# Kernel tuning notes

Measured on AMD Instinct MI355X. Metric: run time of the kernel, lower is better.

Reference implementation:

```python
import jax, jax.numpy as jnp
import numpy as np

BIGINT = 1e10
BOA, BOH, BOL = 21, 22, 23      # global-node residue symbols
ATOM_POS_PAD = 0                # atom position pad index
AG_SEG = 1                      # antigen segment id


def setup_inputs() -> dict:
    key = jax.random.key(0)
    ks = jax.random.split(key, 8)
    B, L, C, E = 16, 128, 14, 256
    N = B * L
    # residues with global tokens at fixed positions per protein
    S = jax.random.randint(ks[0], (B, L), 0, 21)
    S = S.at[:, 0].set(BOA).at[:, 48].set(BOH).at[:, 96].set(BOL)
    S = S.reshape(N)
    seg = np.zeros((L,), np.int32); seg[0:48] = 1; seg[48:96] = 2; seg[96:] = 3
    segment_ids = jnp.tile(jnp.asarray(seg), B)
    RP = jnp.tile(jnp.arange(L, dtype=jnp.int32), B)
    A = jax.random.randint(ks[1], (N, C), 1, 16)
    AP = jax.random.randint(ks[2], (N, C), 0, 16)
    AP = AP.at[:, :4].set(jnp.arange(1, 5, dtype=AP.dtype)[None, :])  # backbone always present
    X = jax.random.normal(ks[3], (N, C, 3), dtype=jnp.float32) * 3.0
    res_embed = jax.random.normal(ks[4], (25, E), dtype=jnp.float32) * 0.02
    atom_embed = jax.random.normal(ks[5], (16, E), dtype=jnp.float32) * 0.02
    atom_pos_embed = jax.random.normal(ks[6], (16, E), dtype=jnp.float32) * 0.02
    return dict(S=S, RP=RP, A=A, AP=AP, X=X, segment_ids=segment_ids,
                res_embed=res_embed, atom_embed=atom_embed,
                atom_pos_embed=atom_pos_embed, max_n=L, k_neighbors=9)


def _embed(S, RP, A, AP, res_embed, atom_embed, atom_pos_embed):
    N = S.shape[0]
    E = res_embed.shape[1]
    half = E // 2
    inv = jnp.power(10000.0, -2.0 * jnp.arange(half, dtype=jnp.float32) / E)
    ang = RP.astype(jnp.float32)[:, None] * inv[None, :]
    pos_e = jnp.stack([jnp.sin(ang), jnp.cos(ang)], axis=-1).reshape(N, E)
    res_e = res_embed[S] + pos_e
    atom_e = atom_embed[A] + atom_pos_embed[AP]            # [N,C,E]
    not_pad = (AP != ATOM_POS_PAD)
    denom = not_pad.sum(-1, keepdims=True).astype(res_e.dtype) + 1e-10
    atom_e = jnp.sum(atom_e * not_pad[..., None], axis=1) / denom
    return jnp.concatenate([res_e, atom_e], axis=-1)       # [N,2E]


def _min_pair_dist(X, AP, max_n):
    # min over atom pairs of ||X[i,a]-X[j,b]||, pad atoms pushed to BIGINT
    N, C, _ = X.shape
    B = N // max_n
    Xb = X.reshape(B, max_n, C, 3)
    pad = (AP == ATOM_POS_PAD).reshape(B, max_n, C)
    sq = jnp.sum(Xb * Xb, axis=-1)                          # [B,L,C]
    dot = jnp.einsum('biad,bjcd->biajc', Xb, Xb)            # [B,L,C,L,C]
    d2 = sq[:, :, :, None, None] + sq[:, None, None, :, :] - 2.0 * dot
    dist = jnp.sqrt(jnp.maximum(d2, 0.0))
    pmask = pad[:, :, :, None, None] | pad[:, None, None, :, :]
    dist = dist + pmask.astype(dist.dtype) * BIGINT
    return jnp.min(dist, axis=(2, 4))                       # [B,L,L]


def _knn(dist_mat, sel_mask, k):
    # smallest-k neighbors among selected candidate edges; invalid -> -1
    B, L, _ = dist_mat.shape
    d = jnp.where(sel_mask, dist_mat, BIGINT)
    neg, dst_local = jax.lax.top_k(-d, k)                   # [B,L,k]
    valid = ((-neg) < BIGINT).reshape(-1)
    offs = (jnp.arange(B) * L)[:, None, None]
    src = jnp.broadcast_to(jnp.arange(L)[None, :, None] + offs, (B, L, k)).reshape(-1)
    dst = (dst_local + offs).reshape(-1)
    src = jnp.where(valid, src, -1)
    dst = jnp.where(valid, dst, -1)
    return jnp.stack([src, dst]), valid


def reference(S, RP, A, AP, X, segment_ids, res_embed, atom_embed, atom_pos_embed, max_n, k_neighbors):
    N = S.shape[0]
    L = max_n
    B = N // L
    h = _embed(S, RP, A, AP, res_embed, atom_embed, atom_pos_embed)
    dist = _min_pair_dist(X, AP, L)                          # [B,L,L]
    g = ((S == BOA) | (S == BOH) | (S == BOL)).reshape(B, L)
    seg = segment_ids.reshape(B, L)
    not_self = ~jnp.eye(L, dtype=bool)[None]                 # exclude i==j
    gi, gj = g[:, :, None], g[:, None, :]
    not_global = ~(gi | gj)
    same_seg = seg[:, :, None] == seg[:, None, :]
    inner_mask = same_seg & not_global & not_self
    outer_mask = (~same_seg) & not_global & not_self
    ctx_knn, ctx_valid = _knn(dist, inner_mask, k_neighbors)
    inter_knn, inter_valid = _knn(dist, outer_mask, k_neighbors)
    # non-kNN ctx edges (global_normal | global_global | sequential), dense adjacency
    global_normal = same_seg & (gi | gj) & not_self
    global_global = gi & gj & not_self
    idx = jnp.arange(L)
    adj_seq = (jnp.abs(idx[:, None] - idx[None, :]) == 1)[None]
    seq_mask = adj_seq & not_global & (seg[:, :, None] != AG_SEG)
    extra_ctx_adj = global_normal | global_global | seq_mask  # [B,L,L] bool
    return h, ctx_knn, ctx_valid, extra_ctx_adj, inter_knn, inter_valid
```

## Files before the change

kernel.cpp:

```cpp
#include <hip/hip_runtime.h>
#include <math.h>
#include <float.h>
#include <stdint.h>

#define BIGINT_F 1e10f
#define L_TOK 128
#define C_ATOM 14
#define E_DIM 256
#define K_NB 9

__device__ __forceinline__ float sq3(float x, float y, float z) {
    return __fadd_rn(__fadd_rn(__fmul_rn(x, x), __fmul_rn(y, y)), __fmul_rn(z, z));
}

__device__ __forceinline__ uint64_t umin64(uint64_t a, uint64_t b) { return a < b ? a : b; }

__global__ void __launch_bounds__(256)
fused_kernel(const int* __restrict__ S, const int* __restrict__ RP,
             const int* __restrict__ A, const int* __restrict__ AP,
             const float* __restrict__ X, const int* __restrict__ seg,
             const float* __restrict__ res_embed,
             const float* __restrict__ atom_embed,
             const float* __restrict__ atom_pos_embed,
             float* __restrict__ h,
             float* __restrict__ ctx_src, float* __restrict__ ctx_dst, float* __restrict__ ctx_val,
             float* __restrict__ adj_out,
             float* __restrict__ int_src, float* __restrict__ int_dst, float* __restrict__ int_val,
             int N) {
    const int NKNN = N / 4;
    int blk = blockIdx.x;
    int tid = threadIdx.x;

    if (blk < NKNN) {
        int wave = tid >> 6;
        int lane = tid & 63;
        int bi = blk * 4 + wave;
        int b  = bi >> 7;
        int i  = bi & (L_TOK - 1);

        __shared__ float4 sxi[4][C_ATOM];
        if (lane < C_ATOM) {
            const float* xp = X + ((size_t)bi * C_ATOM + lane) * 3;
            float x0 = xp[0], x1 = xp[1], x2 = xp[2];
            float sq = (AP[bi * C_ATOM + lane] == 0) ? INFINITY : sq3(x0, x1, x2);
            sxi[wave][lane] = make_float4(x0, x1, x2, sq);
        }
        __syncthreads();

        float xa0[C_ATOM], xa1[C_ATOM], xa2[C_ATOM], sa[C_ATOM];
        #pragma unroll
        for (int a = 0; a < C_ATOM; ++a) {
            float4 t = sxi[wave][a];
            xa0[a] = t.x; xa1[a] = t.y; xa2[a] = t.z; sa[a] = t.w;
        }

        int j0 = lane, j1 = lane + 64;
        int nj0 = (b << 7) + j0, nj1 = (b << 7) + j1;

        float mind0 = INFINITY, mind1 = INFINITY;
        for (int c = 0; c < C_ATOM; ++c) {
            const float* yp0 = X + ((size_t)nj0 * C_ATOM + c) * 3;
            const float* yp1 = X + ((size_t)nj1 * C_ATOM + c) * 3;
            float y00 = yp0[0], y01 = yp0[1], y02 = yp0[2];
            float y10 = yp1[0], y11 = yp1[1], y12 = yp1[2];
            float sc0 = (AP[nj0 * C_ATOM + c] == 0) ? INFINITY : sq3(y00, y01, y02);
            float sc1 = (AP[nj1 * C_ATOM + c] == 0) ? INFINITY : sq3(y10, y11, y12);
            #pragma unroll
            for (int a = 0; a < C_ATOM; ++a) {
                float dot0 = __fadd_rn(__fadd_rn(__fmul_rn(xa0[a], y00),
                                                 __fmul_rn(xa1[a], y01)),
                                       __fmul_rn(xa2[a], y02));
                float d20 = __fsub_rn(__fadd_rn(sa[a], sc0), __fmul_rn(2.0f, dot0));
                mind0 = fminf(mind0, d20);
                float dot1 = __fadd_rn(__fadd_rn(__fmul_rn(xa0[a], y10),
                                                 __fmul_rn(xa1[a], y11)),
                                       __fmul_rn(xa2[a], y12));
                float d21 = __fsub_rn(__fadd_rn(sa[a], sc1), __fmul_rn(2.0f, dot1));
                mind1 = fminf(mind1, d21);
            }
        }
        float d0 = sqrtf(fmaxf(mind0, 0.0f));
        float d1 = sqrtf(fmaxf(mind1, 0.0f));

        int si = S[bi];
        int segi = seg[bi];
        bool gi = si >= 21;
        int sj0 = S[nj0], sj1 = S[nj1];
        int segj0 = seg[nj0], segj1 = seg[nj1];
        bool gj0 = sj0 >= 21, gj1 = sj1 >= 21;
        bool ng0 = !gi && !gj0 && (j0 != i);
        bool ng1 = !gi && !gj1 && (j1 != i);
        bool inner0 = (segi == segj0) && ng0;
        bool inner1 = (segi == segj1) && ng1;
        bool outer0 = (segi != segj0) && ng0;
        bool outer1 = (segi != segj1) && ng1;

        const uint32_t bigbits = __float_as_uint(BIGINT_F);
        uint64_t kd0 = ((uint64_t)__float_as_uint(d0) << 32) | (uint32_t)j0;
        uint64_t kd1 = ((uint64_t)__float_as_uint(d1) << 32) | (uint32_t)j1;
        uint64_t kbig0 = ((uint64_t)bigbits << 32) | (uint32_t)j0;
        uint64_t kbig1 = ((uint64_t)bigbits << 32) | (uint32_t)j1;

        for (int pass = 0; pass < 2; ++pass) {
            uint64_t k0 = (pass == 0 ? inner0 : outer0) ? kd0 : kbig0;
            uint64_t k1 = (pass == 0 ? inner1 : outer1) ? kd1 : kbig1;
            float* osrc = (pass == 0) ? ctx_src : int_src;
            float* odst = (pass == 0) ? ctx_dst : int_dst;
            float* oval = (pass == 0) ? ctx_val : int_val;
            #pragma unroll
            for (int k = 0; k < K_NB; ++k) {
                uint64_t kk = umin64(k0, k1);
                #pragma unroll
                for (int m = 32; m > 0; m >>= 1) {
                    uint64_t o = __shfl_xor((unsigned long long)kk, m, 64);
                    kk = umin64(kk, o);
                }
                if (k0 == kk) k0 = UINT64_MAX;
                if (k1 == kk) k1 = UINT64_MAX;
                if (lane == 0) {
                    uint32_t dbits = (uint32_t)(kk >> 32);
                    int jmin = (int)(uint32_t)kk;
                    bool valid = dbits < bigbits;
                    int o = bi * K_NB + k;
                    osrc[o] = valid ? (float)bi : -1.0f;
                    odst[o] = valid ? (float)((b << 7) + jmin) : -1.0f;
                    oval[o] = valid ? 1.0f : 0.0f;
                }
            }
        }
    } else if (blk < NKNN + N) {
        int n = blk - NKNN;
        int e = tid;
        int s = S[n];
        float rp = (float)RP[n];

        int k = e >> 1;
        const float c1 = (float)(-2.0 * 13.287712379549449 / (double)E_DIM);
        float invk = exp2f((float)k * c1);
        float ang = rp * invk;
        float pe = (e & 1) ? cosf(ang) : sinf(ang);
        h[(size_t)n * (2 * E_DIM) + e] = res_embed[s * E_DIM + e] + pe;

        __shared__ int sA[C_ATOM], sAP[C_ATOM];
        if (e < C_ATOM) { sA[e] = A[n * C_ATOM + e]; sAP[e] = AP[n * C_ATOM + e]; }
        __syncthreads();

        float sum = 0.0f, cnt = 0.0f;
        for (int c = 0; c < C_ATOM; ++c) {
            if (sAP[c] != 0) {
                sum += atom_embed[sA[c] * E_DIM + e] + atom_pos_embed[sAP[c] * E_DIM + e];
                cnt += 1.0f;
            }
        }
        h[(size_t)n * (2 * E_DIM) + E_DIM + e] = sum / (cnt + 1e-10f);
    } else {
        int idx = (blk - NKNN - N) * 256 + tid;
        int b = idx >> 14;
        int i = (idx >> 7) & (L_TOK - 1);
        int j = idx & (L_TOK - 1);
        int ni = (b << 7) + i, nj = (b << 7) + j;
        bool gi = S[ni] >= 21, gj = S[nj] >= 21;
        int segi = seg[ni], segj = seg[nj];
        bool notself = (i != j);
        bool same = (segi == segj);
        bool gn = same && (gi || gj) && notself;
        bool gg = gi && gj && notself;
        int d = i - j;
        bool adjacent = (d == 1 || d == -1);
        bool sm = adjacent && !(gi || gj) && (segi != 1);
        adj_out[idx] = (gn || gg || sm) ? 1.0f : 0.0f;
    }
}

extern "C" void kernel_launch(void* const* d_in, const int* in_sizes, int n_in,
                              void* d_out, int out_size, void* d_ws, size_t ws_size,
                              hipStream_t stream) {
    const int*   S    = (const int*)d_in[0];
    const int*   RP   = (const int*)d_in[1];
    const int*   A    = (const int*)d_in[2];
    const int*   AP   = (const int*)d_in[3];
    const float* X    = (const float*)d_in[4];
    const int*   seg  = (const int*)d_in[5];
    const float* rese = (const float*)d_in[6];
    const float* atme = (const float*)d_in[7];
    const float* atpe = (const float*)d_in[8];

    const int N = in_sizes[0];
    const int B = N / L_TOK;
    float* out = (float*)d_out;

    size_t off = 0;
    float* h_out   = out + off;  off += (size_t)N * 2 * E_DIM;
    float* ctx_src = out + off;  off += (size_t)N * K_NB;
    float* ctx_dst = out + off;  off += (size_t)N * K_NB;
    float* ctx_val = out + off;  off += (size_t)N * K_NB;
    float* adj_out = out + off;  off += (size_t)B * L_TOK * L_TOK;
    float* int_src = out + off;  off += (size_t)N * K_NB;
    float* int_dst = out + off;  off += (size_t)N * K_NB;
    float* int_val = out + off;  off += (size_t)N * K_NB;

    int nknn = N / 4;
    int nadj = (B * L_TOK * L_TOK) / 256;
    int grid = nknn + N + nadj;
    fused_kernel<<<grid, 256, 0, stream>>>(S, RP, A, AP, X, seg, rese, atme, atpe,
                                           h_out, ctx_src, ctx_dst, ctx_val,
                                           adj_out, int_src, int_dst, int_val, N);
}
```

Before: 97.65 us.

## Replace 64-bit shuffle top-k with DPP float min, ballot argmin, interleaved passes

The k-nearest-neighbour selection drops the packed 64-bit key and xor-shuffle reduction in favour of a 32-bit float wave minimum built from DPP row operations, plus readlane and ballot/ctz to find the lowest lane holding that minimum. The inner and outer selections now run interleaved in one loop, and each lane keeps its k-th result so the outputs go out in one coalesced store instead of lane-0 scalar writes. It also folds the -2 factor into the cached query coordinates to save a multiply per atom pair. Ties now break by lane with the j0 half checked before j1, which still picks the lowest index. Entries with non-finite distances get a reconstructed index instead of the old packed one, but those rows are marked invalid anyway.

```diff
diff --git a/kernel.cpp b/kernel.cpp
--- a/kernel.cpp
+++ b/kernel.cpp
@@ -13,7 +13,19 @@
     return __fadd_rn(__fadd_rn(__fmul_rn(x, x), __fmul_rn(y, y)), __fmul_rn(z, z));
 }
 
-__device__ __forceinline__ uint64_t umin64(uint64_t a, uint64_t b) { return a < b ? a : b; }
+__device__ __forceinline__ float wave_min63(float v) {
+#define DPP_MIN(ctrl)                                                         \
+    v = fminf(v, __int_as_float(__builtin_amdgcn_update_dpp(                  \
+            __float_as_int(v), __float_as_int(v), (ctrl), 0xf, 0xf, false)));
+    DPP_MIN(0x111)
+    DPP_MIN(0x112)
+    DPP_MIN(0x114)
+    DPP_MIN(0x118)
+    DPP_MIN(0x142)
+    DPP_MIN(0x143)
+#undef DPP_MIN
+    return v;
+}
 
 __global__ void __launch_bounds__(256)
 fused_kernel(const int* __restrict__ S, const int* __restrict__ RP,
@@ -37,46 +49,47 @@
         int bi = blk * 4 + wave;
         int b  = bi >> 7;
         int i  = bi & (L_TOK - 1);
+        const float INF_F = __int_as_float(0x7f800000);
 
         __shared__ float4 sxi[4][C_ATOM];
         if (lane < C_ATOM) {
             const float* xp = X + ((size_t)bi * C_ATOM + lane) * 3;
             float x0 = xp[0], x1 = xp[1], x2 = xp[2];
-            float sq = (AP[bi * C_ATOM + lane] == 0) ? INFINITY : sq3(x0, x1, x2);
-            sxi[wave][lane] = make_float4(x0, x1, x2, sq);
+            float sq = (AP[bi * C_ATOM + lane] == 0) ? INF_F : sq3(x0, x1, x2);
+            sxi[wave][lane] = make_float4(__fmul_rn(x0, -2.0f),
+                                          __fmul_rn(x1, -2.0f),
+                                          __fmul_rn(x2, -2.0f), sq);
         }
         __syncthreads();
 
-        float xa0[C_ATOM], xa1[C_ATOM], xa2[C_ATOM], sa[C_ATOM];
+        float za0[C_ATOM], za1[C_ATOM], za2[C_ATOM], sa[C_ATOM];
         #pragma unroll
         for (int a = 0; a < C_ATOM; ++a) {
             float4 t = sxi[wave][a];
-            xa0[a] = t.x; xa1[a] = t.y; xa2[a] = t.z; sa[a] = t.w;
+            za0[a] = t.x; za1[a] = t.y; za2[a] = t.z; sa[a] = t.w;
         }
 
         int j0 = lane, j1 = lane + 64;
         int nj0 = (b << 7) + j0, nj1 = (b << 7) + j1;
 
-        float mind0 = INFINITY, mind1 = INFINITY;
+        float mind0 = INF_F, mind1 = INF_F;
         for (int c = 0; c < C_ATOM; ++c) {
             const float* yp0 = X + ((size_t)nj0 * C_ATOM + c) * 3;
             const float* yp1 = X + ((size_t)nj1 * C_ATOM + c) * 3;
             float y00 = yp0[0], y01 = yp0[1], y02 = yp0[2];
             float y10 = yp1[0], y11 = yp1[1], y12 = yp1[2];
-            float sc0 = (AP[nj0 * C_ATOM + c] == 0) ? INFINITY : sq3(y00, y01, y02);
-            float sc1 = (AP[nj1 * C_ATOM + c] == 0) ? INFINITY : sq3(y10, y11, y12);
+            float sc0 = (AP[nj0 * C_ATOM + c] == 0) ? INF_F : sq3(y00, y01, y02);
+            float sc1 = (AP[nj1 * C_ATOM + c] == 0) ? INF_F : sq3(y10, y11, y12);
             #pragma unroll
             for (int a = 0; a < C_ATOM; ++a) {
-                float dot0 = __fadd_rn(__fadd_rn(__fmul_rn(xa0[a], y00),
-                                                 __fmul_rn(xa1[a], y01)),
-                                       __fmul_rn(xa2[a], y02));
-                float d20 = __fsub_rn(__fadd_rn(sa[a], sc0), __fmul_rn(2.0f, dot0));
-                mind0 = fminf(mind0, d20);
-                float dot1 = __fadd_rn(__fadd_rn(__fmul_rn(xa0[a], y10),
-                                                 __fmul_rn(xa1[a], y11)),
-                                       __fmul_rn(xa2[a], y12));
-                float d21 = __fsub_rn(__fadd_rn(sa[a], sc1), __fmul_rn(2.0f, dot1));
-                mind1 = fminf(mind1, d21);
+                float t0 = __fadd_rn(__fadd_rn(__fmul_rn(za0[a], y00),
+                                               __fmul_rn(za1[a], y01)),
+                                     __fmul_rn(za2[a], y02));
+                mind0 = fminf(mind0, __fadd_rn(__fadd_rn(sa[a], sc0), t0));
+                float t1 = __fadd_rn(__fadd_rn(__fmul_rn(za0[a], y10),
+                                               __fmul_rn(za1[a], y11)),
+                                     __fmul_rn(za2[a], y12));
+                mind1 = fminf(mind1, __fadd_rn(__fadd_rn(sa[a], sc1), t1));
             }
         }
         float d0 = sqrtf(fmaxf(mind0, 0.0f));
@@ -95,38 +108,62 @@
         bool outer0 = (segi != segj0) && ng0;
         bool outer1 = (segi != segj1) && ng1;
 
-        const uint32_t bigbits = __float_as_uint(BIGINT_F);
-        uint64_t kd0 = ((uint64_t)__float_as_uint(d0) << 32) | (uint32_t)j0;
-        uint64_t kd1 = ((uint64_t)__float_as_uint(d1) << 32) | (uint32_t)j1;
-        uint64_t kbig0 = ((uint64_t)bigbits << 32) | (uint32_t)j0;
-        uint64_t kbig1 = ((uint64_t)bigbits << 32) | (uint32_t)j1;
-
-        for (int pass = 0; pass < 2; ++pass) {
-            uint64_t k0 = (pass == 0 ? inner0 : outer0) ? kd0 : kbig0;
-            uint64_t k1 = (pass == 0 ? inner1 : outer1) ? kd1 : kbig1;
-            float* osrc = (pass == 0) ? ctx_src : int_src;
-            float* odst = (pass == 0) ? ctx_dst : int_dst;
-            float* oval = (pass == 0) ? ctx_val : int_val;
-            #pragma unroll
-            for (int k = 0; k < K_NB; ++k) {
-                uint64_t kk = umin64(k0, k1);
-                #pragma unroll
-                for (int m = 32; m > 0; m >>= 1) {
-                    uint64_t o = __shfl_xor((unsigned long long)kk, m, 64);
-                    kk = umin64(kk, o);
-                }
-                if (k0 == kk) k0 = UINT64_MAX;
-                if (k1 == kk) k1 = UINT64_MAX;
-                if (lane == 0) {
-                    uint32_t dbits = (uint32_t)(kk >> 32);
-                    int jmin = (int)(uint32_t)kk;
-                    bool valid = dbits < bigbits;
-                    int o = bi * K_NB + k;
-                    osrc[o] = valid ? (float)bi : -1.0f;
-                    odst[o] = valid ? (float)((b << 7) + jmin) : -1.0f;
-                    oval[o] = valid ? 1.0f : 0.0f;
-                }
-            }
+        float cA0 = inner0 ? d0 : INF_F;
+        float cA1 = inner1 ? d1 : INF_F;
+        float cB0 = outer0 ? d0 : INF_F;
+        float cB1 = outer1 ? d1 : INF_F;
+
+        float rsA = -1.0f, rdA = -1.0f, rvA = 0.0f;
+        float rsB = -1.0f, rdB = -1.0f, rvB = 0.0f;
+
+        #pragma unroll
+        for (int k = 0; k < K_NB; ++k) {
+            float mA = wave_min63(fminf(cA0, cA1));
+            float mB = wave_min63(fminf(cB0, cB1));
+            float sAv = __int_as_float(__builtin_amdgcn_readlane(__float_as_int(mA), 63));
+            float sBv = __int_as_float(__builtin_amdgcn_readlane(__float_as_int(mB), 63));
+
+            int jA;
+            unsigned long long ba0 = __ballot(cA0 == sAv);
+            if (ba0) {
+                int l = __builtin_ctzll(ba0);
+                jA = l;
+                if (lane == l) cA0 = INF_F;
+            } else {
+                unsigned long long ba1 = __ballot(cA1 == sAv);
+                int l = __builtin_ctzll(ba1);
+                jA = l + 64;
+                if (lane == l) cA1 = INF_F;
+            }
+            int jB;
+            unsigned long long bb0 = __ballot(cB0 == sBv);
+            if (bb0) {
+                int l = __builtin_ctzll(bb0);
+                jB = l;
+                if (lane == l) cB0 = INF_F;
+            } else {
+                unsigned long long bb1 = __ballot(cB1 == sBv);
+                int l = __builtin_ctzll(bb1);
+                jB = l + 64;
+                if (lane == l) cB1 = INF_F;
+            }
+
+            if (lane == k) {
+                bool okA = sAv < BIGINT_F;
+                rsA = okA ? (float)bi : -1.0f;
+                rdA = okA ? (float)((b << 7) + jA) : -1.0f;
+                rvA = okA ? 1.0f : 0.0f;
+                bool okB = sBv < BIGINT_F;
+                rsB = okB ? (float)bi : -1.0f;
+                rdB = okB ? (float)((b << 7) + jB) : -1.0f;
+                rvB = okB ? 1.0f : 0.0f;
+            }
+        }
+
+        if (lane < K_NB) {
+            int o = bi * K_NB + lane;
+            ctx_src[o] = rsA; ctx_dst[o] = rdA; ctx_val[o] = rvA;
+            int_src[o] = rsB; int_dst[o] = rdB; int_val[o] = rvB;
         }
     } else if (blk < NKNN + N) {
         int n = blk - NKNN;
```

Measured after the change: 97.65 us. No clear change (+0.0%).
